# Kernel optimization log

Measured on AMD Instinct MI355X. Metric: run time of the kernel, lower is better.

Reference implementation:

```python
import jax, jax.numpy as jnp
import numpy as np

N_GRAPHS = 512
N_PER_GRAPH = 1024
N_NODES = N_GRAPHS * N_PER_GRAPH  # 524288
N_EDGES = 4194304
D_FEAT = 256
KEEP_RATIO = 0.5


def setup_inputs() -> dict:
    key = jax.random.key(0)
    k1, k2, k3, k4 = jax.random.split(key, 4)
    edge_index = jax.random.randint(k1, (2, N_EDGES), 0, N_NODES, dtype=jnp.int32)
    adj_vals = jax.random.uniform(k2, (N_EDGES,), dtype=jnp.float32)
    input_feature = jax.random.normal(k3, (N_NODES, D_FEAT), dtype=jnp.float32)
    W = jax.random.normal(k4, (D_FEAT, 1), dtype=jnp.float32) * 0.05
    graph_indicator = (jnp.arange(N_NODES) // N_PER_GRAPH).astype(jnp.int32)
    return dict(edge_index=edge_index, adj_vals=adj_vals,
                input_feature=input_feature, W=W,
                graph_indicator=graph_indicator)


def reference(edge_index, adj_vals, input_feature, W, graph_indicator):
    N = input_feature.shape[0]
    G, n = N_GRAPHS, N_PER_GRAPH
    k = int(KEEP_RATIO * n)
    row, col = edge_index[0], edge_index[1]

    # attn_gcn: support = X @ W ; score = spmm(A, support)
    support = (input_feature @ W)[:, 0]                              # [N]
    attn = jnp.tanh(jax.ops.segment_sum(adj_vals * support[col], row,
                                        num_segments=N))             # [N]

    # top_rank: per-graph top-k (vectorized; all graphs have n nodes)
    scores = attn.reshape(G, n)                                      # [G, n]
    _, idx = jax.lax.top_k(scores, k)                                # [G, k]
    node_idx = (idx + (jnp.arange(G, dtype=idx.dtype) * n)[:, None]).reshape(-1)  # [G*k]

    hidden = input_feature[node_idx] * attn[node_idx][:, None]       # [G*k, D]
    mask_graph_indicator = graph_indicator[node_idx]                 # [G*k]

    # filter_adjacency (faithful to original: mask is NOT applied; self-loops
    # removed, then GCN renormalization D^-1/2 (A+I) D^-1/2, as edge+diag vals)
    nonself = (row != col).astype(input_feature.dtype)
    deg = jax.ops.segment_sum(nonself, row, num_segments=N) + 1.0    # +I
    inv_sqrt = jax.lax.rsqrt(deg)
    edge_norm = nonself * inv_sqrt[row] * inv_sqrt[col]              # [E]
    diag_norm = 1.0 / deg                                            # [N]

    return hidden, mask_graph_indicator, edge_norm, diag_norm
```

## Files before the change

### kernel.cpp

```cpp
#include <hip/hip_runtime.h>
#include <math.h>

#define N_GRAPHS 512
#define N_PER    1024
#define NN       (N_GRAPHS * N_PER)
#define NE       4194304
#define DF       256
#define KK       512
#define GK       (N_GRAPHS * KK)

#define FIX_SCALE 1073741824.0
#define BIAS_F    32.0f
#define BIAS_FIX  (1ll << 35)
#define CNT_SHIFT 50
#define LOW_MASK  ((1ull << CNT_SHIFT) - 1)

#define NB   512
#define B1   512
#define T1   512
#define CHUNK (NE / B1)
#define BCAP 64

__global__ void k_init(unsigned long long* __restrict__ acc,
                       unsigned int* __restrict__ selfcnt) {
    int i = blockIdx.x * blockDim.x + threadIdx.x;
    if (i < NN) { acc[i] = 0ull; selfcnt[i] = 0u; }
}

__global__ void k_support(const float* __restrict__ X, const float* __restrict__ W,
                          float* __restrict__ support) {
    __shared__ float sW[DF];
    int t = threadIdx.x;
    sW[t] = W[t];
    __syncthreads();
    int wv = t >> 6, lane = t & 63;
    int row = blockIdx.x * 4 + wv;
    const float4 x = ((const float4*)(X + (size_t)row * DF))[lane];
    const float4 w = ((const float4*)sW)[lane];
    float s = x.x * w.x + x.y * w.y + x.z * w.z + x.w * w.w;
    #pragma unroll
    for (int off = 32; off; off >>= 1) s += __shfl_down(s, off, 64);
    if (lane == 0) support[row] = s;
}

__global__ void k_bin(const int* __restrict__ row, const int* __restrict__ col,
                      const float* __restrict__ adj, const float* __restrict__ support,
                      uint2* __restrict__ recs, unsigned int* __restrict__ cnts,
                      unsigned int* __restrict__ selfcnt) {
    __shared__ uint2        rec[CHUNK];
    __shared__ unsigned int cnt[NB];
    __shared__ unsigned int ls[NB];
    __shared__ unsigned int cur[NB];
    int t = threadIdx.x;
    int blk = blockIdx.x;
    int base = blk * CHUNK;

    cnt[t] = 0u;
    __syncthreads();

    #pragma unroll
    for (int k = 0; k < CHUNK / T1; ++k) {
        int r = row[base + k * T1 + t];
        atomicAdd(&cnt[r >> 10], 1u);
    }
    __syncthreads();

    ls[t] = cnt[t];
    __syncthreads();
    for (int off = 1; off < NB; off <<= 1) {
        unsigned int add = (t >= off) ? ls[t - off] : 0u;
        __syncthreads();
        ls[t] += add;
        __syncthreads();
    }
    ls[t] -= cnt[t];
    cur[t] = ls[t];
    cnts[(size_t)t * B1 + blk] = cnt[t];
    __syncthreads();

    #pragma unroll
    for (int k = 0; k < CHUNK / T1; ++k) {
        int e = base + k * T1 + t;
        int r = row[e], c = col[e];
        float term = adj[e] * support[c];
        unsigned int ns = (r != c) ? 1u : 0u;
        if (!ns) atomicAdd(&selfcnt[r], 1u);
        unsigned int pos = atomicAdd(&cur[r >> 10], 1u);
        rec[pos] = make_uint2((unsigned int)r | (ns << 31), __float_as_uint(term));
    }
    __syncthreads();

    for (int j = t; j < CHUNK; j += T1) {
        uint2 u = rec[j];
        unsigned int b = (u.x & 0x7FFFFFFFu) >> 10;
        unsigned int local = j - ls[b];
        if (local < BCAP)
            recs[((size_t)b * B1 + blk) * BCAP + local] = u;
    }
}

__global__ void k_accum(const uint2* __restrict__ recs,
                        const unsigned int* __restrict__ cnts,
                        unsigned long long* __restrict__ acc) {
    __shared__ unsigned long long lacc[N_PER];
    int t = threadIdx.x;
    int b = blockIdx.x;
    #pragma unroll
    for (int k = 0; k < N_PER / 256; ++k) lacc[t + k * 256] = 0ull;
    __syncthreads();

    for (int blk = t; blk < B1; blk += 256) {
        unsigned int n = cnts[(size_t)b * B1 + blk];
        if (n > BCAP) n = BCAP;
        const uint2* p = recs + ((size_t)b * B1 + blk) * BCAP;
        for (unsigned int i = 0; i < n; ++i) {
            uint2 u = p[i];
            unsigned int lr = u.x & (N_PER - 1);
            unsigned long long ns = (unsigned long long)(u.x >> 31);
            float term = __uint_as_float(u.y);
            term = fminf(fmaxf(term, -BIAS_F), BIAS_F);
            long long f = llrint((double)term * FIX_SCALE);
            atomicAdd(&lacc[lr], (ns << CNT_SHIFT) + (unsigned long long)(f + BIAS_FIX));
        }
    }
    __syncthreads();
    #pragma unroll
    for (int k = 0; k < N_PER / 256; ++k)
        acc[(size_t)b * N_PER + t + k * 256] = lacc[t + k * 256];
}

__global__ void k_scatter(const int* __restrict__ row, const int* __restrict__ col,
                          const float* __restrict__ adj, const float* __restrict__ support,
                          unsigned long long* __restrict__ acc,
                          unsigned int* __restrict__ selfcnt) {
    int e = blockIdx.x * blockDim.x + threadIdx.x;
    if (e >= NE) return;
    int r = row[e], c = col[e];
    float term = adj[e] * support[c];
    term = fminf(fmaxf(term, -BIAS_F), BIAS_F);
    long long f = llrint((double)term * FIX_SCALE);
    unsigned long long contrib =
        ((unsigned long long)(r != c) << CNT_SHIFT) +
        (unsigned long long)(f + BIAS_FIX);
    atomicAdd(&acc[r], contrib);
    if (r == c) atomicAdd(&selfcnt[r], 1u);
}

__global__ void k_finalize(const unsigned long long* __restrict__ acc,
                           unsigned int* __restrict__ self_then_rs,
                           float* __restrict__ attn, float* __restrict__ diag) {
    int i = blockIdx.x * blockDim.x + threadIdx.x;
    if (i >= NN) return;
    unsigned long long a = acc[i];
    unsigned int cnt = (unsigned int)(a >> CNT_SHIFT);
    unsigned long long low = a & LOW_MASK;
    unsigned int selfc = self_then_rs[i];
    long long sfix = (long long)low
                   - ((long long)(cnt + selfc) << 35);
    float sum = (float)((double)sfix * (1.0 / FIX_SCALE));
    attn[i] = tanhf(sum);
    float degf = (float)(1u + cnt);
    diag[i] = 1.0f / degf;
    ((float*)self_then_rs)[i] = rsqrtf(degf);
}

__global__ void k_topk(const float* __restrict__ attn, int* __restrict__ nidx) {
    __shared__ float sv[N_PER];
    __shared__ int   si[N_PER];
    int g = blockIdx.x, t = threadIdx.x;
    int base = g * N_PER;
    sv[t] = attn[base + t];
    si[t] = t;
    __syncthreads();
    for (int k = 2; k <= N_PER; k <<= 1) {
        for (int j = k >> 1; j > 0; j >>= 1) {
            int l = t ^ j;
            if (l > t) {
                float v1 = sv[t], v2 = sv[l];
                int   i1 = si[t], i2 = si[l];
                bool cmp_l_t = (v2 > v1) || (v2 == v1 && i2 < i1);
                bool swap = ((t & k) == 0) ? cmp_l_t : !cmp_l_t;
                if (swap) { sv[t] = v2; si[t] = i2; sv[l] = v1; si[l] = i1; }
            }
            __syncthreads();
        }
    }
    if (t < KK) nidx[g * KK + t] = base + si[t];
}

__global__ void k_gather(const float* __restrict__ X, const float* __restrict__ attn,
                         const int* __restrict__ nidx, const int* __restrict__ gi,
                         float* __restrict__ hidden, float* __restrict__ mask) {
    int t = threadIdx.x;
    int wv = t >> 6, lane = t & 63;
    int r = blockIdx.x * 4 + wv;
    int node = nidx[r];
    float a = attn[node];
    float4 x = ((const float4*)(X + (size_t)node * DF))[lane];
    x.x *= a; x.y *= a; x.z *= a; x.w *= a;
    ((float4*)(hidden + (size_t)r * DF))[lane] = x;
    if (lane == 0) mask[r] = (float)gi[node];
}

__global__ void k_edgenorm(const int* __restrict__ row, const int* __restrict__ col,
                           const float* __restrict__ rs, float* __restrict__ en) {
    int e = blockIdx.x * blockDim.x + threadIdx.x;
    if (e >= NE) return;
    int r = row[e], c = col[e];
    en[e] = (r != c) ? rs[r] * rs[c] : 0.0f;
}

extern "C" void kernel_launch(void* const* d_in, const int* in_sizes, int n_in,
                              void* d_out, int out_size, void* d_ws, size_t ws_size,
                              hipStream_t stream) {
    const int*   edge_index = (const int*)d_in[0];
    const float* adj_vals   = (const float*)d_in[1];
    const float* X          = (const float*)d_in[2];
    const float* W          = (const float*)d_in[3];
    const int*   gi         = (const int*)d_in[4];

    const int* row = edge_index;
    const int* col = edge_index + NE;

    float* out_hidden = (float*)d_out;
    float* out_mask   = out_hidden + (size_t)GK * DF;
    float* out_edge   = out_mask + GK;
    float* out_diag   = out_edge + NE;

    const size_t MB = 1024 * 1024;
    char* ws = (char*)d_ws;
    float*              support = (float*)ws;
    unsigned int*       selfrs  = (unsigned int*)(ws + 2 * MB);
    float*              attn    = (float*)(ws + 4 * MB);
    int*                nidx    = (int*)(ws + 6 * MB);
    unsigned int*       cnts    = (unsigned int*)(ws + 7 * MB);
    unsigned long long* acc     = (unsigned long long*)(ws + 8 * MB);
    uint2*              recs    = (uint2*)(ws + 12 * MB);
    const size_t need = 12 * MB + (size_t)NB * B1 * BCAP * sizeof(uint2);

    k_init<<<NN / 256, 256, 0, stream>>>(acc, selfrs);
    k_support<<<NN / 4, 256, 0, stream>>>(X, W, support);
    if (ws_size >= need) {
        k_bin<<<B1, T1, 0, stream>>>(row, col, adj_vals, support, recs, cnts, selfrs);
        k_accum<<<NB, 256, 0, stream>>>(recs, cnts, acc);
    } else {
        k_scatter<<<NE / 256, 256, 0, stream>>>(row, col, adj_vals, support, acc, selfrs);
    }
    k_finalize<<<NN / 256, 256, 0, stream>>>(acc, selfrs, attn, out_diag);
    k_topk<<<N_GRAPHS, N_PER, 0, stream>>>(attn, nidx);
    k_gather<<<GK / 4, 256, 0, stream>>>(X, attn, nidx, gi, out_hidden, out_mask);
    k_edgenorm<<<NE / 256, 256, 0, stream>>>(row, col, (const float*)selfrs, out_edge);
}
```

Measured before the change: 988.2 us.

## Drop binning prefix scan and fuse finalize and top-k sort into accumulate kernel

The binning kernel no longer counts and prefix-scans its chunk or stages records in shared memory. It writes each record directly to a per-(block, bucket) slot using a shared atomic cursor, with layout transposed to blk-major. The accumulate kernel now uses 512 threads (one per source block), then does finalize (tanh, degree, diag, rsqrt) and a packed 64-bit-key bitonic sort per graph in shared memory. It emits the top-k indices and the selected attention values, which removes the acc round trip, the finalize and topk launches and the attn reloads. The cost is scattered global writes from the binning kernel in place of coalesced ones.

```diff
diff --git a/kernel.cpp b/kernel.cpp
--- a/kernel.cpp
+++ b/kernel.cpp
@@ -24,7 +24,7 @@
 __global__ void k_init(unsigned long long* __restrict__ acc,
                        unsigned int* __restrict__ selfcnt) {
     int i = blockIdx.x * blockDim.x + threadIdx.x;
-    if (i < NN) { acc[i] = 0ull; selfcnt[i] = 0u; }
+    if (i < NN) { selfcnt[i] = 0u; if (acc) acc[i] = 0ull; }
 }
 
 __global__ void k_support(const float* __restrict__ X, const float* __restrict__ W,
@@ -47,37 +47,12 @@
                       const float* __restrict__ adj, const float* __restrict__ support,
                       uint2* __restrict__ recs, unsigned int* __restrict__ cnts,
                       unsigned int* __restrict__ selfcnt) {
-    __shared__ uint2        rec[CHUNK];
-    __shared__ unsigned int cnt[NB];
-    __shared__ unsigned int ls[NB];
     __shared__ unsigned int cur[NB];
     int t = threadIdx.x;
     int blk = blockIdx.x;
     int base = blk * CHUNK;
-
-    cnt[t] = 0u;
-    __syncthreads();
-
-    #pragma unroll
-    for (int k = 0; k < CHUNK / T1; ++k) {
-        int r = row[base + k * T1 + t];
-        atomicAdd(&cnt[r >> 10], 1u);
-    }
-    __syncthreads();
-
-    ls[t] = cnt[t];
-    __syncthreads();
-    for (int off = 1; off < NB; off <<= 1) {
-        unsigned int add = (t >= off) ? ls[t - off] : 0u;
-        __syncthreads();
-        ls[t] += add;
-        __syncthreads();
-    }
-    ls[t] -= cnt[t];
-    cur[t] = ls[t];
-    cnts[(size_t)t * B1 + blk] = cnt[t];
-    __syncthreads();
-
+    cur[t] = 0u;
+    __syncthreads();
     #pragma unroll
     for (int k = 0; k < CHUNK / T1; ++k) {
         int e = base + k * T1 + t;
@@ -85,48 +60,101 @@
         float term = adj[e] * support[c];
         unsigned int ns = (r != c) ? 1u : 0u;
         if (!ns) atomicAdd(&selfcnt[r], 1u);
-        unsigned int pos = atomicAdd(&cur[r >> 10], 1u);
-        rec[pos] = make_uint2((unsigned int)r | (ns << 31), __float_as_uint(term));
-    }
-    __syncthreads();
-
-    for (int j = t; j < CHUNK; j += T1) {
-        uint2 u = rec[j];
-        unsigned int b = (u.x & 0x7FFFFFFFu) >> 10;
-        unsigned int local = j - ls[b];
-        if (local < BCAP)
-            recs[((size_t)b * B1 + blk) * BCAP + local] = u;
-    }
-}
-
-__global__ void k_accum(const uint2* __restrict__ recs,
-                        const unsigned int* __restrict__ cnts,
-                        unsigned long long* __restrict__ acc) {
+        unsigned int b = (unsigned int)r >> 10;
+        unsigned int pos = atomicAdd(&cur[b], 1u);
+        if (pos < BCAP)
+            recs[((size_t)blk * NB + b) * BCAP + pos] =
+                make_uint2((unsigned int)r | (ns << 31), __float_as_uint(term));
+    }
+    __syncthreads();
+    cnts[blk * NB + t] = cur[t];
+}
+
+__global__ __launch_bounds__(512)
+void k_accum(const uint2* __restrict__ recs, const unsigned int* __restrict__ cnts,
+             unsigned int* __restrict__ self_then_rs, float* __restrict__ diag,
+             float* __restrict__ attn_sel, int* __restrict__ nidx) {
     __shared__ unsigned long long lacc[N_PER];
     int t = threadIdx.x;
     int b = blockIdx.x;
+    lacc[t] = 0ull; lacc[t + 512] = 0ull;
+    __syncthreads();
+
+    unsigned int n = cnts[(size_t)t * NB + b];
+    if (n > BCAP) n = BCAP;
+    const uint2* p = recs + ((size_t)t * NB + b) * BCAP;
+    for (unsigned int i = 0; i < n; ++i) {
+        uint2 u = p[i];
+        unsigned int lr = u.x & (N_PER - 1);
+        unsigned long long ns = (unsigned long long)(u.x >> 31);
+        float term = __uint_as_float(u.y);
+        term = fminf(fmaxf(term, -BIAS_F), BIAS_F);
+        long long f = llrint((double)term * FIX_SCALE);
+        atomicAdd(&lacc[lr], (ns << CNT_SHIFT) + (unsigned long long)(f + BIAS_FIX));
+    }
+    __syncthreads();
+
+    int gbase = b * N_PER;
     #pragma unroll
-    for (int k = 0; k < N_PER / 256; ++k) lacc[t + k * 256] = 0ull;
-    __syncthreads();
-
-    for (int blk = t; blk < B1; blk += 256) {
-        unsigned int n = cnts[(size_t)b * B1 + blk];
-        if (n > BCAP) n = BCAP;
-        const uint2* p = recs + ((size_t)b * B1 + blk) * BCAP;
-        for (unsigned int i = 0; i < n; ++i) {
-            uint2 u = p[i];
-            unsigned int lr = u.x & (N_PER - 1);
-            unsigned long long ns = (unsigned long long)(u.x >> 31);
-            float term = __uint_as_float(u.y);
-            term = fminf(fmaxf(term, -BIAS_F), BIAS_F);
-            long long f = llrint((double)term * FIX_SCALE);
-            atomicAdd(&lacc[lr], (ns << CNT_SHIFT) + (unsigned long long)(f + BIAS_FIX));
+    for (int h = 0; h < 2; ++h) {
+        int i = t + h * 512;
+        unsigned long long a = lacc[i];
+        unsigned int cnt = (unsigned int)(a >> CNT_SHIFT);
+        unsigned long long low = a & LOW_MASK;
+        unsigned int selfc = self_then_rs[gbase + i];
+        long long sfix = (long long)low
+                       - ((long long)(cnt + selfc) << 35);
+        float sum = (float)((double)sfix * (1.0 / FIX_SCALE));
+        float av = tanhf(sum);
+        float degf = (float)(1u + cnt);
+        diag[gbase + i] = 1.0f / degf;
+        ((float*)self_then_rs)[gbase + i] = rsqrtf(degf);
+        unsigned int bv  = __float_as_uint(av);
+        unsigned int ord = (bv & 0x80000000u) ? ~bv : (bv | 0x80000000u);
+        lacc[i] = ((unsigned long long)ord << 10)
+                | (unsigned long long)(N_PER - 1 - i);
+    }
+    __syncthreads();
+
+    for (int k = 2; k <= N_PER; k <<= 1) {
+        for (int j = k >> 1; j > 0; j >>= 1) {
+            int i = ((t & ~(j - 1)) << 1) | (t & (j - 1));
+            int l = i | j;
+            unsigned long long a0 = lacc[i], a1 = lacc[l];
+            bool up = ((i & k) == 0);
+            if ((a0 < a1) == up) { lacc[i] = a1; lacc[l] = a0; }
+            __syncthreads();
         }
     }
-    __syncthreads();
-    #pragma unroll
-    for (int k = 0; k < N_PER / 256; ++k)
-        acc[(size_t)b * N_PER + t + k * 256] = lacc[t + k * 256];
+
+    unsigned long long key = lacc[t];
+    unsigned int idx = N_PER - 1 - (unsigned int)(key & (N_PER - 1));
+    unsigned int ord = (unsigned int)(key >> 10);
+    unsigned int bv  = (ord & 0x80000000u) ? (ord ^ 0x80000000u) : ~ord;
+    nidx[b * KK + t]     = gbase + (int)idx;
+    attn_sel[b * KK + t] = __uint_as_float(bv);
+}
+
+__global__ void k_gather(const float* __restrict__ X, const float* __restrict__ attn_sel,
+                         const int* __restrict__ nidx, const int* __restrict__ gi,
+                         float* __restrict__ hidden, float* __restrict__ mask) {
+    int t = threadIdx.x;
+    int wv = t >> 6, lane = t & 63;
+    int r = blockIdx.x * 4 + wv;
+    int node = nidx[r];
+    float a = attn_sel[r];
+    float4 x = ((const float4*)(X + (size_t)node * DF))[lane];
+    x.x *= a; x.y *= a; x.z *= a; x.w *= a;
+    ((float4*)(hidden + (size_t)r * DF))[lane] = x;
+    if (lane == 0) mask[r] = (float)gi[node];
+}
+
+__global__ void k_edgenorm(const int* __restrict__ row, const int* __restrict__ col,
+                           const float* __restrict__ rs, float* __restrict__ en) {
+    int e = blockIdx.x * blockDim.x + threadIdx.x;
+    if (e >= NE) return;
+    int r = row[e], c = col[e];
+    en[e] = (r != c) ? rs[r] * rs[c] : 0.0f;
 }
 
 __global__ void k_scatter(const int* __restrict__ row, const int* __restrict__ col,
@@ -155,8 +183,7 @@
     unsigned int cnt = (unsigned int)(a >> CNT_SHIFT);
     unsigned long long low = a & LOW_MASK;
     unsigned int selfc = self_then_rs[i];
-    long long sfix = (long long)low
-                   - ((long long)(cnt + selfc) << 35);
+    long long sfix = (long long)low - ((long long)(cnt + selfc) << 35);
     float sum = (float)((double)sfix * (1.0 / FIX_SCALE));
     attn[i] = tanhf(sum);
     float degf = (float)(1u + cnt);
@@ -188,9 +215,9 @@
     if (t < KK) nidx[g * KK + t] = base + si[t];
 }
 
-__global__ void k_gather(const float* __restrict__ X, const float* __restrict__ attn,
-                         const int* __restrict__ nidx, const int* __restrict__ gi,
-                         float* __restrict__ hidden, float* __restrict__ mask) {
+__global__ void k_gather_fb(const float* __restrict__ X, const float* __restrict__ attn,
+                            const int* __restrict__ nidx, const int* __restrict__ gi,
+                            float* __restrict__ hidden, float* __restrict__ mask) {
     int t = threadIdx.x;
     int wv = t >> 6, lane = t & 63;
     int r = blockIdx.x * 4 + wv;
@@ -202,14 +229,6 @@
     if (lane == 0) mask[r] = (float)gi[node];
 }
 
-__global__ void k_edgenorm(const int* __restrict__ row, const int* __restrict__ col,
-                           const float* __restrict__ rs, float* __restrict__ en) {
-    int e = blockIdx.x * blockDim.x + threadIdx.x;
-    if (e >= NE) return;
-    int r = row[e], c = col[e];
-    en[e] = (r != c) ? rs[r] * rs[c] : 0.0f;
-}
-
 extern "C" void kernel_launch(void* const* d_in, const int* in_sizes, int n_in,
                               void* d_out, int out_size, void* d_ws, size_t ws_size,
                               hipStream_t stream) {
@@ -229,25 +248,28 @@
 
     const size_t MB = 1024 * 1024;
     char* ws = (char*)d_ws;
-    float*              support = (float*)ws;
-    unsigned int*       selfrs  = (unsigned int*)(ws + 2 * MB);
-    float*              attn    = (float*)(ws + 4 * MB);
-    int*                nidx    = (int*)(ws + 6 * MB);
-    unsigned int*       cnts    = (unsigned int*)(ws + 7 * MB);
-    unsigned long long* acc     = (unsigned long long*)(ws + 8 * MB);
-    uint2*              recs    = (uint2*)(ws + 12 * MB);
-    const size_t need = 12 * MB + (size_t)NB * B1 * BCAP * sizeof(uint2);
-
-    k_init<<<NN / 256, 256, 0, stream>>>(acc, selfrs);
+    float*              support  = (float*)ws;
+    unsigned int*       selfrs   = (unsigned int*)(ws + 2 * MB);
+    float*              attn     = (float*)(ws + 4 * MB);
+    int*                nidx     = (int*)(ws + 6 * MB);
+    unsigned int*       cnts     = (unsigned int*)(ws + 7 * MB);
+    unsigned long long* acc      = (unsigned long long*)(ws + 8 * MB);
+    float*              attn_sel = (float*)(ws + 12 * MB);
+    uint2*              recs     = (uint2*)(ws + 13 * MB);
+    const size_t need = 13 * MB + (size_t)NB * B1 * BCAP * sizeof(uint2);
+
     k_support<<<NN / 4, 256, 0, stream>>>(X, W, support);
     if (ws_size >= need) {
+        k_init<<<NN / 256, 256, 0, stream>>>((unsigned long long*)nullptr, selfrs);
         k_bin<<<B1, T1, 0, stream>>>(row, col, adj_vals, support, recs, cnts, selfrs);
-        k_accum<<<NB, 256, 0, stream>>>(recs, cnts, acc);
+        k_accum<<<NB, 512, 0, stream>>>(recs, cnts, selfrs, out_diag, attn_sel, nidx);
+        k_gather<<<GK / 4, 256, 0, stream>>>(X, attn_sel, nidx, gi, out_hidden, out_mask);
     } else {
+        k_init<<<NN / 256, 256, 0, stream>>>(acc, selfrs);
         k_scatter<<<NE / 256, 256, 0, stream>>>(row, col, adj_vals, support, acc, selfrs);
-    }
-    k_finalize<<<NN / 256, 256, 0, stream>>>(acc, selfrs, attn, out_diag);
-    k_topk<<<N_GRAPHS, N_PER, 0, stream>>>(attn, nidx);
-    k_gather<<<GK / 4, 256, 0, stream>>>(X, attn, nidx, gi, out_hidden, out_mask);
+        k_finalize<<<NN / 256, 256, 0, stream>>>(acc, selfrs, attn, out_diag);
+        k_topk<<<N_GRAPHS, N_PER, 0, stream>>>(attn, nidx);
+        k_gather_fb<<<GK / 4, 256, 0, stream>>>(X, attn, nidx, gi, out_hidden, out_mask);
+    }
     k_edgenorm<<<NE / 256, 256, 0, stream>>>(row, col, (const float*)selfrs, out_edge);
 }
```

New measurement: 1.034 ms. 1.05x slower.
